# Kernel optimization log

Measured on AMD Instinct MI355X. Metric: run time of the kernel, lower is better.

The kernel has to match this reference:

```python
import jax, jax.numpy as jnp
import numpy as np

NEG_SLOPE = 0.2

def gat_conv(x, src, dst, W, a_src, a_dst, b, num_nodes, concat):
    # PyG GATConv (add_self_loops already applied to src/dst).
    H, C = a_src.shape
    h = (x @ W).reshape(-1, H, C)                      # [N,H,C]
    s = jnp.einsum('nhc,hc->nh', h, a_src)             # per-node src score
    d = jnp.einsum('nhc,hc->nh', h, a_dst)             # per-node dst score
    e = jax.nn.leaky_relu(s[src] + d[dst], NEG_SLOPE)  # [E,H]
    emax = jax.lax.stop_gradient(
        jax.ops.segment_max(e, dst, num_segments=num_nodes))  # [N,H]
    ex = jnp.exp(e - emax[dst])
    denom = jax.ops.segment_sum(ex, dst, num_segments=num_nodes)
    alpha = ex / denom[dst]                            # segment softmax over in-edges
    msg = h[src] * alpha[:, :, None]                   # [E,H,C]
    out = jax.ops.segment_sum(msg, dst, num_segments=num_nodes)
    out = out.reshape(num_nodes, H * C) if concat else out.mean(axis=1)
    return out + b

def setup_inputs() -> dict:
    key = jax.random.key(0)
    ks = jax.random.split(key, 20)
    N, E, F = 50000, 400000, 256
    x = jax.random.normal(ks[0], (N, F), dtype=jnp.float32)
    edge_index = jax.random.randint(ks[1], (2, E), 0, N, dtype=jnp.int64)
    def p(k, shape):
        return (jax.random.normal(k, shape, dtype=jnp.float32) * 0.1)
    inp = {'x': x, 'edge_index': edge_index}
    # conv1: 256 -> 8x32 ; conv2: 256 -> 4x32 ; conv3: 128 -> 2x32 ; conv4: 64 -> 1x32
    dims = [(256, 8, 32), (256, 4, 32), (128, 2, 32), (64, 1, 32)]
    ki = 2
    for i, (fin, H, C) in enumerate(dims, start=1):
        inp[f'W{i}'] = p(ks[ki], (fin, H * C)); ki += 1
        inp[f'a_src{i}'] = p(ks[ki], (H, C)); ki += 1
        inp[f'a_dst{i}'] = p(ks[ki], (H, C)); ki += 1
        bdim = H * C if i < 4 else C
        inp[f'b{i}'] = jnp.zeros((bdim,), dtype=jnp.float32)
    return inp

def reference(x, edge_index, W1, a_src1, a_dst1, b1, W2, a_src2, a_dst2, b2,
              W3, a_src3, a_dst3, b3, W4, a_src4, a_dst4, b4):
    N = x.shape[0]
    loops = jnp.arange(N, dtype=edge_index.dtype)
    src = jnp.concatenate([edge_index[0], loops])
    dst = jnp.concatenate([edge_index[1], loops])
    h = jax.nn.elu(gat_conv(x, src, dst, W1, a_src1, a_dst1, b1, N, True))
    h = jax.nn.elu(gat_conv(h, src, dst, W2, a_src2, a_dst2, b2, N, True))
    h = gat_conv(h, src, dst, W3, a_src3, a_dst3, b3, N, True)
    h = jax.nn.elu(h)
    h = gat_conv(h, src, dst, W4, a_src4, a_dst4, b4, N, False)
    return jax.nn.log_softmax(h, axis=1)
```

## Files before the change

### kernel.cpp

```cpp
#include <hip/hip_runtime.h>
#include <hip/hip_bf16.h>

#define LRELU_SLOPE 0.2f

typedef __attribute__((ext_vector_type(8))) short short8;
typedef __attribute__((ext_vector_type(4))) float f32x4;

__device__ __forceinline__ unsigned short bf16r(float f) {
    unsigned int u = __builtin_bit_cast(unsigned int, f);
    u += 0x7fffu + ((u >> 16) & 1u);
    return (unsigned short)(u >> 16);
}
__device__ __forceinline__ float bf2f(unsigned short u) {
    return __builtin_bit_cast(float, (unsigned int)u << 16);
}

#define GLD16(g, l)                                                            \
    __builtin_amdgcn_global_load_lds(                                          \
        (const __attribute__((address_space(1))) void*)(g),                    \
        (__attribute__((address_space(3))) void*)(l), 16, 0, 0)


#define WTOT 108544

__global__ void k_pre(const float* __restrict__ x, unsigned short* __restrict__ Xb,
                      const float* __restrict__ Wa, const float* __restrict__ Wb,
                      const float* __restrict__ Wc, const float* __restrict__ Wd,
                      unsigned short* __restrict__ Ta, unsigned short* __restrict__ Tb,
                      unsigned short* __restrict__ Tc, unsigned short* __restrict__ Td,
                      const int* __restrict__ ei, int* __restrict__ cnt,
                      int* __restrict__ slot, int XC, int E) {
    int gid = blockIdx.x * blockDim.x + threadIdx.x;
    if (gid < XC) {
        const float4* xp = (const float4*)x + (long)gid * 2;
        float4 a = xp[0], b = xp[1];
        short8 pk;
        pk[0] = (short)bf16r(a.x); pk[1] = (short)bf16r(a.y);
        pk[2] = (short)bf16r(a.z); pk[3] = (short)bf16r(a.w);
        pk[4] = (short)bf16r(b.x); pk[5] = (short)bf16r(b.y);
        pk[6] = (short)bf16r(b.z); pk[7] = (short)bf16r(b.w);
        *(short8*)(Xb + (long)gid * 8) = pk;
        return;
    }
    int id = gid - XC;
    if (id < WTOT) {
        const float* W; unsigned short* T; int K, Nc;
        if (id < 65536)       { W = Wa; T = Ta; K = 256; Nc = 256; }
        else if (id < 98304)  { id -= 65536;  W = Wb; T = Tb; K = 256; Nc = 128; }
        else if (id < 106496) { id -= 98304;  W = Wc; T = Tc; K = 128; Nc = 64; }
        else                  { id -= 106496; W = Wd; T = Td; K = 64;  Nc = 32; }
        int n = id / K, k = id % K;
        T[id] = bf16r(W[(long)k * Nc + n]);
        return;
    }
    int e = id - WTOT;
    if (e >= E) return;
    int dst = ei[E + e];
    slot[e] = atomicAdd(&cnt[dst], 1);
}


__global__ void k_scan_blk(const int* __restrict__ cnt, int* __restrict__ offs,
                           int* __restrict__ bsum, int* __restrict__ bpre,
                           int* __restrict__ done, int N, int NB) {
    __shared__ int temp[1024];
    __shared__ int last_s;
    int t = threadIdx.x;
    int gi = blockIdx.x * 1024 + t;
    int v = (gi < N) ? cnt[gi] + 1 : 0;
    temp[t] = v;
    __syncthreads();
    for (int o = 1; o < 1024; o <<= 1) {
        int x = (t >= o) ? temp[t - o] : 0;
        __syncthreads();
        temp[t] += x;
        __syncthreads();
    }
    if (gi < N) offs[gi] = temp[t] - v;
    if (t == 1023) bsum[blockIdx.x] = temp[1023];
    if (t == 0) {
        __threadfence();
        last_s = (atomicAdd(done, 1) == NB - 1) ? 1 : 0;
    }
    __syncthreads();
    if (last_s) {
        __threadfence();
        int v2 = (t < NB) ? bsum[t] : 0;
        temp[t] = v2;
        __syncthreads();
        for (int o = 1; o < 1024; o <<= 1) {
            int x = (t >= o) ? temp[t - o] : 0;
            __syncthreads();
            temp[t] += x;
            __syncthreads();
        }
        if (t < NB) bpre[t] = temp[t] - v2;
        if (t == NB - 1) bpre[NB] = temp[t];
    }
}

__global__ void k_scan_add(int* __restrict__ offs, const int* __restrict__ bpre,
                           int* __restrict__ adj, int N, int nb) {
    int gi = blockIdx.x * blockDim.x + threadIdx.x;
    if (gi < N) {
        int v = offs[gi] + bpre[gi >> 10];
        offs[gi] = v;
        adj[v] = gi;
    } else if (gi == N) {
        offs[N] = bpre[nb];
    }
}

__global__ void k_scatter(const int* __restrict__ ei, const int* __restrict__ offs,
                          const int* __restrict__ slot, int* __restrict__ adj, int E) {
    int e = blockIdx.x * blockDim.x + threadIdx.x;
    if (e >= E) return;
    int srcn = ei[e];
    int dst  = ei[E + e];
    adj[offs[dst] + 1 + slot[e]] = srcn;
}


template<int BN, int KT, int GX>
__global__ __launch_bounds__(256) void k_mgemm(const unsigned short* __restrict__ Ab,
                                               const unsigned short* __restrict__ WT,
                                               unsigned short* __restrict__ Cb,
                                               const float* __restrict__ a_src,
                                               const float* __restrict__ a_dst,
                                               float* __restrict__ sbuf,
                                               float* __restrict__ dbuf,
                                               int M, int Nc, int H, int RB) {
    constexpr int KITER = KT / 32;
    constexpr int NBF = BN / 16;
    constexpr int CPR = BN / 32;
    constexpr int SP  = BN + 8;
    constexpr int ASH = 64 * KT;
    constexpr int BSH = BN * KT;
    constexpr int EPIL = 64 * SP;
    constexpr int LBSZ = (ASH + BSH) > EPIL ? (ASH + BSH) : EPIL;
    constexpr int SHC = (KT == 256) ? 5 : (KT == 128 ? 4 : 3);
    constexpr int BIT = BN * KT / 2048;
    __shared__ __align__(16) unsigned short LB[LBSZ];

    int id = blockIdx.x;
    int xcd = id & 7;
    int q  = id >> 3;
    int ct = q % GX;
    int rb = (q / GX) * 8 + xcd;
    if (rb >= RB) return;
    int bm = rb * 64, bn = ct * BN;

    int t = threadIdx.x;
    int wv = t >> 6, l = t & 63;
    int row_in = l & 15, quad = l >> 4;
    char* LBb = (char*)LB;

    long abyte = (long)bm * (KT * 2);
    long mbyte = (long)M * (KT * 2);
    const char* Agb = (const char*)Ab;
#pragma unroll
    for (int i = 0; i < KITER; ++i) {
        int c = i * 256 + t;
        int cs = c ^ ((c >> SHC) & 7);
        long gb = abyte + (long)cs * 16;
        if (gb >= mbyte) gb = abyte;
        GLD16(Agb + gb, LBb + (i * 256 + wv * 64) * 16);
    }
    const char* WTb = (const char*)WT + (long)bn * (KT * 2);
#pragma unroll
    for (int i = 0; i < BIT; ++i) {
        int c = i * 256 + t;
        int cs = c ^ ((c >> SHC) & 7);
        GLD16(WTb + (long)cs * 16, LBb + ASH * 2 + (i * 256 + wv * 64) * 16);
    }
    asm volatile("s_waitcnt vmcnt(0)" ::: "memory");
    __syncthreads();

    f32x4 acc[NBF];
#pragma unroll
    for (int j = 0; j < NBF; ++j) acc[j] = (f32x4){0.f, 0.f, 0.f, 0.f};

    int arow = wv * 16 + row_in;
#pragma unroll
    for (int ki = 0; ki < KITER; ++ki) {
        int aoff = (arow * (KT * 2) + ki * 64 + quad * 16) ^ ((arow & 7) << 4);
        short8 av = *(const short8*)(LBb + aoff);
#pragma unroll
        for (int f = 0; f < NBF; ++f) {
            int bcol = f * 16 + row_in;
            int boff = ASH * 2 + ((bcol * (KT * 2) + ki * 64 + quad * 16) ^ ((bcol & 7) << 4));
            short8 bv = *(const short8*)(LBb + boff);
            acc[f] = __builtin_amdgcn_mfma_f32_16x16x32_bf16(av, bv, acc[f], 0, 0, 0);
        }
    }
    __syncthreads();

#pragma unroll
    for (int r = 0; r < 4; ++r)
#pragma unroll
        for (int f = 0; f < NBF; ++f)
            LB[(wv * 16 + quad * 4 + r) * SP + f * 16 + row_in] = bf16r(acc[f][r]);
    __syncthreads();

    int rr = t / CPR, cc = t % CPR;
    if (rr < 64) {
        int grow = bm + rr;
        int colb = bn + cc * 32;
        if (grow < M && colb < Nc) {
            const unsigned short* ep = &LB[rr * SP + cc * 32];
            short8 v0 = *(const short8*)(ep);
            short8 v1 = *(const short8*)(ep + 8);
            short8 v2 = *(const short8*)(ep + 16);
            short8 v3 = *(const short8*)(ep + 24);
            unsigned short* cp = &Cb[(long)grow * Nc + colb];
            *(short8*)(cp)      = v0;
            *(short8*)(cp + 8)  = v1;
            *(short8*)(cp + 16) = v2;
            *(short8*)(cp + 24) = v3;
            int hd = colb >> 5;
            const float* ap = a_src + hd * 32;
            const float* dp = a_dst + hd * 32;
            float ss = 0.f, dd = 0.f;
#pragma unroll
            for (int u = 0; u < 8; ++u) {
                float va = bf2f((unsigned short)v0[u]); ss += va * ap[u];      dd += va * dp[u];
                float vb = bf2f((unsigned short)v1[u]); ss += vb * ap[8 + u];  dd += vb * dp[8 + u];
                float vc = bf2f((unsigned short)v2[u]); ss += vc * ap[16 + u]; dd += vc * dp[16 + u];
                float vd = bf2f((unsigned short)v3[u]); ss += vd * ap[24 + u]; dd += vd * dp[24 + u];
            }
            sbuf[(long)grow * H + hd] = ss;
            dbuf[(long)grow * H + hd] = dd;
        }
    }
}


#define QB(v, k) __builtin_amdgcn_ds_swizzle((v), 0x8000 | ((k) * 0x55))

template<int ACT>
__global__ void k_aggf(const unsigned short* __restrict__ h, const float* __restrict__ s,
                       const float* __restrict__ dsc, const int* __restrict__ offs,
                       const int* __restrict__ adj, const float* __restrict__ bias,
                       unsigned short* __restrict__ out16, float* __restrict__ out32,
                       int N, int H) {
    const int C8 = 4;
    long tid = (long)blockIdx.x * blockDim.x + threadIdx.x;
    int HC8 = H * C8;
    if (tid >= (long)N * HC8) return;
    int c8 = (int)(tid % C8);
    int hh = (int)((tid / C8) % H);
    int n  = (int)(tid / HC8);
    int beg = offs[n], end = offs[n + 1];
    float dn = dsc[n * H + hh];
    int HC = HC8 * 8;
    int coff = hh * 32 + c8 * 8;
    const unsigned short* hb = h + coff;

    float denom = 0.f;
    float acc[8];
#pragma unroll
    for (int u = 0; u < 8; ++u) acc[u] = 0.f;

    for (int j = beg; j < end; j += 4) {
        int my = j + c8;
        int idx = my < end ? my : end - 1;
        int sn = adj[idx];
        float e = s[sn * H + hh] + dn;
        e = e > 0.f ? e : LRELU_SLOPE * e;
        float w = __expf(fminf(e, 80.f));
        if (my >= end) w = 0.f;
        int wi = __builtin_bit_cast(int, w);
        int sn0 = QB(sn, 0);
        int sn1 = QB(sn, 1);
        int sn2 = QB(sn, 2);
        int sn3 = QB(sn, 3);
        float w0 = __builtin_bit_cast(float, QB(wi, 0));
        float w1 = __builtin_bit_cast(float, QB(wi, 1));
        float w2 = __builtin_bit_cast(float, QB(wi, 2));
        float w3 = __builtin_bit_cast(float, QB(wi, 3));
        short8 h0 = *(const short8*)(hb + (size_t)sn0 * HC);
        short8 h1 = *(const short8*)(hb + (size_t)sn1 * HC);
        short8 h2 = *(const short8*)(hb + (size_t)sn2 * HC);
        short8 h3 = *(const short8*)(hb + (size_t)sn3 * HC);
        denom += (w0 + w1) + (w2 + w3);
#pragma unroll
        for (int u = 0; u < 8; ++u) {
            float a01 = w0 * bf2f((unsigned short)h0[u]) + w1 * bf2f((unsigned short)h1[u]);
            float a23 = w2 * bf2f((unsigned short)h2[u]) + w3 * bf2f((unsigned short)h3[u]);
            acc[u] += a01 + a23;
        }
    }

    float inv = 1.0f / denom;
    float o[8];
#pragma unroll
    for (int u = 0; u < 8; ++u) o[u] = acc[u] * inv + bias[coff + u];

    if (ACT == 1) {
        short8 pk;
#pragma unroll
        for (int u = 0; u < 8; ++u) {
            float v = o[u] > 0.f ? o[u] : (__expf(o[u]) - 1.f);
            pk[u] = (short)bf16r(v);
        }
        *(short8*)(out16 + tid * 8) = pk;
    } else {
        float m = o[0];
#pragma unroll
        for (int u = 1; u < 8; ++u) m = fmaxf(m, o[u]);
        m = fmaxf(m, __shfl_xor(m, 1));
        m = fmaxf(m, __shfl_xor(m, 2));
        float ssum = 0.f;
#pragma unroll
        for (int u = 0; u < 8; ++u) ssum += __expf(o[u] - m);
        ssum += __shfl_xor(ssum, 1);
        ssum += __shfl_xor(ssum, 2);
        float lse = m + __logf(ssum);
        float4 lo = {o[0] - lse, o[1] - lse, o[2] - lse, o[3] - lse};
        float4 hi = {o[4] - lse, o[5] - lse, o[6] - lse, o[7] - lse};
        *(float4*)(out32 + tid * 8)     = lo;
        *(float4*)(out32 + tid * 8 + 4) = hi;
    }
}


static inline size_t align_up(size_t x) { return (x + 255) & ~(size_t)255; }

extern "C" void kernel_launch(void* const* d_in, const int* in_sizes, int n_in,
                              void* d_out, int out_size, void* d_ws, size_t ws_size,
                              hipStream_t stream) {
    const float* x   = (const float*)d_in[0];
    const int*   ei  = (const int*)d_in[1];

    const int N = in_sizes[0] / 256;
    const int E = in_sizes[1] / 2;
    const int ET = E + N;
    const int NB = (N + 1023) / 1024;
    const int XC = N * 32;

    size_t off = 0;
    char* ws = (char*)d_ws;
    auto take = [&](size_t bytes) { char* p = ws + off; off += align_up(bytes); return p; };
    int*   offs  = (int*)take((size_t)(N + 1) * 4);
    int*   cntd  = (int*)take((size_t)(N + 1) * 4);
    int*   slot  = (int*)take((size_t)E * 4);
    int*   adj   = (int*)take((size_t)ET * 4);
    int*   bsum  = (int*)take((size_t)(NB + 1) * 4);
    int*   bpre  = (int*)take((size_t)(NB + 1) * 4);
    float* sbuf  = (float*)take((size_t)N * 8 * 4);
    float* dbuf  = (float*)take((size_t)N * 8 * 4);
    unsigned short* Xb = (unsigned short*)take((size_t)N * 256 * 2);
    unsigned short* Yb = (unsigned short*)take((size_t)N * 256 * 2);
    unsigned short* WT0 = (unsigned short*)take((size_t)256 * 256 * 2);
    unsigned short* WT1 = (unsigned short*)take((size_t)256 * 128 * 2);
    unsigned short* WT2 = (unsigned short*)take((size_t)128 * 64 * 2);
    unsigned short* WT3 = (unsigned short*)take((size_t)64 * 32 * 2);
    (void)ws_size;

    int* cnt  = cntd;
    int* done = cntd + N;

    hipMemsetAsync(cntd, 0, (size_t)(N + 1) * 4, stream);
    {
        long tot = (long)XC + WTOT + E;
        k_pre<<<(int)((tot + 255) / 256), 256, 0, stream>>>(
            x, Xb,
            (const float*)d_in[2], (const float*)d_in[6], (const float*)d_in[10],
            (const float*)d_in[14], WT0, WT1, WT2, WT3, ei, cnt, slot, XC, E);
        k_scan_blk<<<NB, 1024, 0, stream>>>(cnt, offs, bsum, bpre, done, N, NB);
        k_scan_add<<<(N + 256) / 256, 256, 0, stream>>>(offs, bpre, adj, N, NB);
        k_scatter<<<(E + 255) / 256, 256, 0, stream>>>(ei, offs, slot, adj, E);
    }

    const float* as_[4] = {(const float*)d_in[3], (const float*)d_in[7],
                           (const float*)d_in[11], (const float*)d_in[15]};
    const float* ad_[4] = {(const float*)d_in[4], (const float*)d_in[8],
                           (const float*)d_in[12], (const float*)d_in[16]};
    const float* b_[4]  = {(const float*)d_in[5], (const float*)d_in[9],
                           (const float*)d_in[13], (const float*)d_in[17]};
    int H_[4] = {8, 4, 2, 1};

    const int RB  = (N + 63) / 64;
    const int RBp = ((RB + 7) / 8) * 8;

    for (int li = 0; li < 4; ++li) {
        int H = H_[li];

        if (li == 0) {
            k_mgemm<64, 256, 4><<<4 * RBp, 256, 0, stream>>>(
                Xb, WT0, Yb, as_[0], ad_[0], sbuf, dbuf, N, 256, H, RB);
        } else if (li == 1) {
            k_mgemm<64, 256, 2><<<2 * RBp, 256, 0, stream>>>(
                Xb, WT1, Yb, as_[1], ad_[1], sbuf, dbuf, N, 128, H, RB);
        } else if (li == 2) {
            k_mgemm<64, 128, 1><<<RBp, 256, 0, stream>>>(
                Xb, WT2, Yb, as_[2], ad_[2], sbuf, dbuf, N, 64, H, RB);
        } else {
            k_mgemm<32, 64, 1><<<RBp, 256, 0, stream>>>(
                Xb, WT3, Yb, as_[3], ad_[3], sbuf, dbuf, N, 32, H, RB);
        }
        {
            long total = (long)N * H * 4;
            int nb = (int)((total + 255) / 256);
            if (li < 3)
                k_aggf<1><<<nb, 256, 0, stream>>>(Yb, sbuf, dbuf, offs, adj, b_[li],
                                                  Xb, nullptr, N, H);
            else
                k_aggf<0><<<nb, 256, 0, stream>>>(Yb, sbuf, dbuf, offs, adj, b_[li],
                                                  nullptr, (float*)d_out, N, H);
        }
    }
}
```

Baseline: 308.5 us.

## Fuse scan-add with edge scatter and split K=256 GEMM into two LDS rounds

The scan-add and edge-scatter kernels become one finalize kernel. Edges compute their CSR offset directly from the raw block-local scan plus the block prefix, kept in a separate offsR buffer, which saves a launch and a dependency. The bf16 GEMM for K=256 now stages A and B in two K-halves of 128, which halves the LDS footprint so more blocks can be resident per CU. The cost is an extra barrier and a serialized load-then-compute round per half, with no overlap between the two rounds.

```diff
diff --git a/kernel.cpp b/kernel.cpp
--- a/kernel.cpp
+++ b/kernel.cpp
@@ -60,7 +60,7 @@
 }
 
 
-__global__ void k_scan_blk(const int* __restrict__ cnt, int* __restrict__ offs,
+__global__ void k_scan_blk(const int* __restrict__ cnt, int* __restrict__ offsR,
                            int* __restrict__ bsum, int* __restrict__ bpre,
                            int* __restrict__ done, int N, int NB) {
     __shared__ int temp[1024];
@@ -76,7 +76,7 @@
         temp[t] += x;
         __syncthreads();
     }
-    if (gi < N) offs[gi] = temp[t] - v;
+    if (gi < N) offsR[gi] = temp[t] - v;
     if (t == 1023) bsum[blockIdx.x] = temp[1023];
     if (t == 0) {
         __threadfence();
@@ -99,25 +99,28 @@
     }
 }
 
-__global__ void k_scan_add(int* __restrict__ offs, const int* __restrict__ bpre,
-                           int* __restrict__ adj, int N, int nb) {
+
+__global__ void k_finalize(const int* __restrict__ ei, const int* __restrict__ offsR,
+                           const int* __restrict__ bpre, const int* __restrict__ slot,
+                           int* __restrict__ offs, int* __restrict__ adj,
+                           int N, int NB, int E) {
     int gi = blockIdx.x * blockDim.x + threadIdx.x;
-    if (gi < N) {
-        int v = offs[gi] + bpre[gi >> 10];
-        offs[gi] = v;
-        adj[v] = gi;
-    } else if (gi == N) {
-        offs[N] = bpre[nb];
-    }
-}
-
-__global__ void k_scatter(const int* __restrict__ ei, const int* __restrict__ offs,
-                          const int* __restrict__ slot, int* __restrict__ adj, int E) {
-    int e = blockIdx.x * blockDim.x + threadIdx.x;
+    int NA = (N + 256) & ~255;
+    if (gi < NA) {
+        if (gi < N) {
+            int v = offsR[gi] + bpre[gi >> 10];
+            offs[gi] = v;
+            adj[v] = gi;
+        } else if (gi == N) {
+            offs[N] = bpre[NB];
+        }
+        return;
+    }
+    int e = gi - NA;
     if (e >= E) return;
     int srcn = ei[e];
     int dst  = ei[E + e];
-    adj[offs[dst] + 1 + slot[e]] = srcn;
+    adj[offsR[dst] + bpre[dst >> 10] + 1 + slot[e]] = srcn;
 }
 
 
@@ -130,16 +133,20 @@
                                                float* __restrict__ sbuf,
                                                float* __restrict__ dbuf,
                                                int M, int Nc, int H, int RB) {
-    constexpr int KITER = KT / 32;
+    constexpr int KH   = (KT == 256) ? 128 : KT;
+    constexpr int NR   = KT / KH;
+    constexpr int KITER = KH / 32;
     constexpr int NBF = BN / 16;
     constexpr int CPR = BN / 32;
     constexpr int SP  = BN + 8;
-    constexpr int ASH = 64 * KT;
-    constexpr int BSH = BN * KT;
+    constexpr int ASH = 64 * KH;
+    constexpr int BSH = BN * KH;
     constexpr int EPIL = 64 * SP;
     constexpr int LBSZ = (ASH + BSH) > EPIL ? (ASH + BSH) : EPIL;
-    constexpr int SHC = (KT == 256) ? 5 : (KT == 128 ? 4 : 3);
-    constexpr int BIT = BN * KT / 2048;
+    constexpr int CHR = KH / 8;
+    constexpr int SHC = (KH == 128) ? 4 : 3;
+    constexpr int AIT = CHR / 4;
+    constexpr int BIT = BN * CHR / 256;
     __shared__ __align__(16) unsigned short LB[LBSZ];
 
     int id = blockIdx.x;
@@ -155,42 +162,52 @@
     int row_in = l & 15, quad = l >> 4;
     char* LBb = (char*)LB;
 
-    long abyte = (long)bm * (KT * 2);
-    long mbyte = (long)M * (KT * 2);
     const char* Agb = (const char*)Ab;
-#pragma unroll
-    for (int i = 0; i < KITER; ++i) {
-        int c = i * 256 + t;
-        int cs = c ^ ((c >> SHC) & 7);
-        long gb = abyte + (long)cs * 16;
-        if (gb >= mbyte) gb = abyte;
-        GLD16(Agb + gb, LBb + (i * 256 + wv * 64) * 16);
-    }
-    const char* WTb = (const char*)WT + (long)bn * (KT * 2);
-#pragma unroll
-    for (int i = 0; i < BIT; ++i) {
-        int c = i * 256 + t;
-        int cs = c ^ ((c >> SHC) & 7);
-        GLD16(WTb + (long)cs * 16, LBb + ASH * 2 + (i * 256 + wv * 64) * 16);
-    }
-    asm volatile("s_waitcnt vmcnt(0)" ::: "memory");
-    __syncthreads();
+    const char* WTb = (const char*)WT;
 
     f32x4 acc[NBF];
 #pragma unroll
     for (int j = 0; j < NBF; ++j) acc[j] = (f32x4){0.f, 0.f, 0.f, 0.f};
 
     int arow = wv * 16 + row_in;
-#pragma unroll
-    for (int ki = 0; ki < KITER; ++ki) {
-        int aoff = (arow * (KT * 2) + ki * 64 + quad * 16) ^ ((arow & 7) << 4);
-        short8 av = *(const short8*)(LBb + aoff);
-#pragma unroll
-        for (int f = 0; f < NBF; ++f) {
-            int bcol = f * 16 + row_in;
-            int boff = ASH * 2 + ((bcol * (KT * 2) + ki * 64 + quad * 16) ^ ((bcol & 7) << 4));
-            short8 bv = *(const short8*)(LBb + boff);
-            acc[f] = __builtin_amdgcn_mfma_f32_16x16x32_bf16(av, bv, acc[f], 0, 0, 0);
+
+#pragma unroll
+    for (int r = 0; r < NR; ++r) {
+        if (r > 0) __syncthreads();
+
+#pragma unroll
+        for (int i = 0; i < AIT; ++i) {
+            int c = i * 256 + t;
+            int row = c >> SHC;
+            int ci  = c & (CHR - 1);
+            int cis = ci ^ (row & 7);
+            int grow = bm + row; if (grow >= M) grow = M - 1;
+            long gb = (long)grow * (KT * 2) + r * (KH * 2) + cis * 16;
+            GLD16(Agb + gb, LBb + (i * 256 + wv * 64) * 16);
+        }
+#pragma unroll
+        for (int i = 0; i < BIT; ++i) {
+            int c = i * 256 + t;
+            int col = c >> SHC;
+            int ci  = c & (CHR - 1);
+            int cis = ci ^ (col & 7);
+            long gb = (long)(bn + col) * (KT * 2) + r * (KH * 2) + cis * 16;
+            GLD16(WTb + gb, LBb + ASH * 2 + (i * 256 + wv * 64) * 16);
+        }
+        asm volatile("s_waitcnt vmcnt(0)" ::: "memory");
+        __syncthreads();
+
+#pragma unroll
+        for (int ki = 0; ki < KITER; ++ki) {
+            int aoff = (arow * (KH * 2) + ki * 64 + quad * 16) ^ ((arow & 7) << 4);
+            short8 av = *(const short8*)(LBb + aoff);
+#pragma unroll
+            for (int f = 0; f < NBF; ++f) {
+                int bcol = f * 16 + row_in;
+                int boff = ASH * 2 + ((bcol * (KH * 2) + ki * 64 + quad * 16) ^ ((bcol & 7) << 4));
+                short8 bv = *(const short8*)(LBb + boff);
+                acc[f] = __builtin_amdgcn_mfma_f32_16x16x32_bf16(av, bv, acc[f], 0, 0, 0);
+            }
         }
     }
     __syncthreads();
@@ -342,6 +359,7 @@
     char* ws = (char*)d_ws;
     auto take = [&](size_t bytes) { char* p = ws + off; off += align_up(bytes); return p; };
     int*   offs  = (int*)take((size_t)(N + 1) * 4);
+    int*   offsR = (int*)take((size_t)(N + 1) * 4);
     int*   cntd  = (int*)take((size_t)(N + 1) * 4);
     int*   slot  = (int*)take((size_t)E * 4);
     int*   adj   = (int*)take((size_t)ET * 4);
@@ -367,9 +385,10 @@
             x, Xb,
             (const float*)d_in[2], (const float*)d_in[6], (const float*)d_in[10],
             (const float*)d_in[14], WT0, WT1, WT2, WT3, ei, cnt, slot, XC, E);
-        k_scan_blk<<<NB, 1024, 0, stream>>>(cnt, offs, bsum, bpre, done, N, NB);
-        k_scan_add<<<(N + 256) / 256, 256, 0, stream>>>(offs, bpre, adj, N, NB);
-        k_scatter<<<(E + 255) / 256, 256, 0, stream>>>(ei, offs, slot, adj, E);
+        k_scan_blk<<<NB, 1024, 0, stream>>>(cnt, offsR, bsum, bpre, done, N, NB);
+        int NA = (N + 256) & ~255;
+        k_finalize<<<(NA + E + 255) / 256, 256, 0, stream>>>(
+            ei, offsR, bpre, slot, offs, adj, N, NB, E);
     }
 
     const float* as_[4] = {(const float*)d_in[3], (const float*)d_in[7],
```

New measurement: 294.8 us. 4.5% less time.
